# Kernel optimization log

Measured on AMD Instinct MI355X. Metric: run time of the kernel, lower is better.

## Reference

```python
import jax, jax.numpy as jnp
import numpy as np

N = 1024
D = 256            # model_dims
H = D // 2         # hidden_dim = 128
L = 3              # num_levels
EPS = 1e-5


def ln(x, g, b):
    mu = jnp.mean(x, axis=-1, keepdims=True)
    v = jnp.mean((x - mu) ** 2, axis=-1, keepdims=True)
    return (x - mu) / jnp.sqrt(v + EPS) * g + b


def setup_inputs() -> dict:
    key = jax.random.key(0)
    ks = jax.random.split(key, 24)
    s = 0.02
    inp = {
        'atomic_numbers': jax.random.randint(ks[0], (N,), 0, 100),
        'positions': jax.random.normal(ks[1], (N, 3), dtype=jnp.float32) * 3.0,
        'emb': jax.random.normal(ks[2], (100, H), dtype=jnp.float32) * s,
        # distance_expansion: Linear(3, H) + SiLU + LayerNorm(H)
        'de_W': jax.random.normal(ks[3], (L, H), dtype=jnp.float32) * s,
        'de_b': jnp.zeros((H,), jnp.float32),
        'de_g': jnp.ones((H,), jnp.float32),
        'de_be': jnp.zeros((H,), jnp.float32),
        'msg_W': jax.random.normal(ks[4], (L, 2 * H, H), dtype=jnp.float32) * s,
        'msg_b': jnp.zeros((L, H), jnp.float32),
        'msg_g': jnp.ones((L, H), jnp.float32),
        'msg_be': jnp.zeros((L, H), jnp.float32),
        'upd_W': jax.random.normal(ks[5], (L, 2 * H, H), dtype=jnp.float32) * s,
        'upd_b': jnp.zeros((L, H), jnp.float32),
        'upd_g': jnp.ones((L, H), jnp.float32),
        'upd_be': jnp.zeros((L, H), jnp.float32),
        # final proj: Linear(3H, D) + LayerNorm(D)
        'fp_W': jax.random.normal(ks[6], (L * H, D), dtype=jnp.float32) * s,
        'fp_b': jnp.zeros((D,), jnp.float32),
        'fp_g': jnp.ones((D,), jnp.float32),
        'fp_be': jnp.zeros((D,), jnp.float32),
    }
    return inp


def reference(atomic_numbers, positions, emb, de_W, de_b, de_g, de_be,
              msg_W, msg_b, msg_g, msg_be, upd_W, upd_b, upd_g, upd_be,
              fp_W, fp_b, fp_g, fp_be):
    x = emb[atomic_numbers]                                    # [N,H]
    diff = positions[:, None, :] - positions[None, :, :]       # [N,N,3]
    sq = jnp.sum(diff * diff, axis=-1)
    d = jnp.where(sq > 0, jnp.sqrt(jnp.where(sq > 0, sq, 1.0)), 0.0)  # safe norm
    scales = jnp.stack([jnp.exp(-d), jnp.exp(-d / 2), jnp.exp(-d / 4)], axis=-1)  # [N,N,3]
    ew = ln(jax.nn.silu(scales @ de_W + de_b), de_g, de_be)    # [N,N,H]

    level_feats = []
    for lvl in range(L):
        Wi, Wj = msg_W[lvl, :H], msg_W[lvl, H:]
        # cat([x_i, x_j]) @ W == x_i @ Wi + x_j @ Wj
        pre = x @ Wi                                           # [N,H]
        prj = x @ Wj                                           # [N,H]
        m = ln(jax.nn.silu(pre[:, None, :] + prj[None, :, :] + msg_b[lvl]),
               msg_g[lvl], msg_be[lvl])                        # [N,N,H]
        msum = jnp.einsum('ijh,ijh->ih', m, ew)                # sum over j
        u = jnp.concatenate([x, msum], axis=-1)                # [N,2H]
        x = x + ln(jax.nn.silu(u @ upd_W[lvl] + upd_b[lvl]), upd_g[lvl], upd_be[lvl])
        level_feats.append(jnp.mean(x, axis=0))

    combined = jnp.concatenate(level_feats, axis=0)            # [3H]
    return ln(combined @ fp_W + fp_b, fp_g, fp_be)             # [D]
```

## Files before the change

kernel.cpp:

```cpp
#include <hip/hip_runtime.h>
#include <math.h>

constexpr int N_ = 1024;
constexpr int H_ = 128;
constexpr int D_ = 256;
constexpr int L_ = 3;
constexpr float EPS_ = 1e-5f;
constexpr float LOG2E_ = 1.44269504f;
constexpr int KLUT_ = 4096;
constexpr float DMAX_ = 40.0f;
constexpr float TSCALE_ = (KLUT_ - 1) / DMAX_;
constexpr float TMAX_ = (float)(KLUT_ - 1) - 0.001f;

__device__ __forceinline__ float fsig(float v) {
    float e = __builtin_amdgcn_exp2f(v * -LOG2E_);
    return __builtin_amdgcn_rcpf(1.0f + e);
}

template <int CTRL>
__device__ __forceinline__ float rowadd(float x) {
    int y = __builtin_amdgcn_update_dpp(0, __float_as_int(x), CTRL, 0xF, 0xF, true);
    return x + __int_as_float(y);
}
__device__ __forceinline__ float rowreduce16(float x) {
    x = rowadd<0x128>(x);
    x = rowadd<0x124>(x);
    x = rowadd<0x122>(x);
    x = rowadd<0x121>(x);
    return x;
}

__device__ __forceinline__ unsigned bfr(float x) {
    unsigned u = __float_as_uint(x);
    return (u + 0x7FFFu + ((u >> 16) & 1u)) >> 16;
}

#define LD8(dst, src)                                                     \
    {                                                                     \
        float4 t0_ = *(const float4*)(src);                               \
        float4 t1_ = *(const float4*)((src) + 4);                         \
        dst[0] = t0_.x; dst[1] = t0_.y; dst[2] = t0_.z; dst[3] = t0_.w;   \
        dst[4] = t1_.x; dst[5] = t1_.y; dst[6] = t1_.z; dst[7] = t1_.w;   \
    }

__global__ void k_lut(const float* __restrict__ deW, const float* __restrict__ deb,
                      const float* __restrict__ deg, const float* __restrict__ debe,
                      unsigned* __restrict__ lutp) {
    int e = blockIdx.x * 4 + (threadIdx.x >> 6);
    int lane = threadIdx.x & 63;
    float res[2][2];
#pragma unroll
    for (int t = 0; t < 2; ++t) {
        int ee = min(e + t, KLUT_ - 1);
        float d = ee * (DMAX_ / (KLUT_ - 1));
        float s0 = expf(-d), s1 = expf(-0.5f * d), s2 = expf(-0.25f * d);
        float v[2];
        float sum = 0.f, ssq = 0.f;
#pragma unroll
        for (int kk = 0; kk < 2; ++kk) {
            int c = lane + 64 * kk;
            float a = s0 * deW[c] + s1 * deW[H_ + c] + s2 * deW[2 * H_ + c] + deb[c];
            float sg = 1.f / (1.f + expf(-a));
            v[kk] = a * sg;
            sum += v[kk]; ssq += v[kk] * v[kk];
        }
#pragma unroll
        for (int mask = 1; mask < 64; mask <<= 1) {
            sum += __shfl_xor(sum, mask);
            ssq += __shfl_xor(ssq, mask);
        }
        float mu = sum * (1.f / H_);
        float var = ssq * (1.f / H_) - mu * mu;
        float rstd = 1.f / sqrtf(var + EPS_);
#pragma unroll
        for (int kk = 0; kk < 2; ++kk) {
            int c = lane + 64 * kk;
            res[t][kk] = (v[kk] - mu) * rstd * deg[c] + debe[c];
        }
    }
#pragma unroll
    for (int kk = 0; kk < 2; ++kk) {
        int c = lane + 64 * kk;
        lutp[e * H_ + c] = bfr(res[0][kk]) | (bfr(res[1][kk] - res[0][kk]) << 16);
    }
}

__global__ void k_embed_gemm(const int* __restrict__ an, const float* __restrict__ emb,
                             const float* __restrict__ W, const float* __restrict__ b,
                             float* __restrict__ x, float* __restrict__ preb,
                             float* __restrict__ prj) {
    int i = blockIdx.x;
    int t = threadIdx.x;
    __shared__ float xr[H_];
    if (t < H_) {
        float xv = emb[an[i] * H_ + t];
        xr[t] = xv;
        x[i * H_ + t] = xv;
    }
    __syncthreads();
    int h = t & (H_ - 1);
    int off = (t >= H_) ? H_ : 0;
    float s = 0.f;
#pragma unroll 4
    for (int k = 0; k < H_; k += 4) {
        float4 xv = *(const float4*)&xr[k];
        s = fmaf(xv.x, W[(off + k) * H_ + h], s);
        s = fmaf(xv.y, W[(off + k + 1) * H_ + h], s);
        s = fmaf(xv.z, W[(off + k + 2) * H_ + h], s);
        s = fmaf(xv.w, W[(off + k + 3) * H_ + h], s);
    }
    if (t >= H_) prj[i * H_ + h] = s;
    else         preb[i * H_ + h] = s + b[h];
}

__device__ __forceinline__ void prf_step(int JT, int p, int cb, const int2* jinfo,
                                         const unsigned* __restrict__ lutp,
                                         const float* __restrict__ prjR,
                                         unsigned (&LW)[8], float (&TM)[8], float& FR) {
    int jw = (JT & (N_ - 1)) + p;
    int2 ji = jinfo[jw];
    FR = __int_as_float(ji.y);
    const unsigned* lp = (const unsigned*)((const char*)lutp + ji.x) + cb;
    uint4 a = *(const uint4*)lp;
    uint4 b = *(const uint4*)(lp + 4);
    LW[0] = a.x; LW[1] = a.y; LW[2] = a.z; LW[3] = a.w;
    LW[4] = b.x; LW[5] = b.y; LW[6] = b.z; LW[7] = b.w;
    LD8(TM, prjR + jw * H_ + cb);
}

__device__ __forceinline__ void cmp_step(const unsigned (&LW)[8], float (&TM)[8], float FR,
                                         const float (&pbv)[8], const float (&mgv)[8],
                                         const float (&mbev)[8], float (&acc)[8]) {
    float sum = 0.f, ssq = 0.f;
#pragma unroll
    for (int k = 0; k < 8; ++k) {
        float v = pbv[k] + TM[k];
        v *= fsig(v);
        TM[k] = v; sum += v; ssq = fmaf(v, v, ssq);
    }
    sum = rowreduce16(sum);
    ssq = rowreduce16(ssq);
    float mu = sum * (1.f / H_);
    float var = fmaf(ssq, 1.f / H_, -mu * mu);
    float rstd = __builtin_amdgcn_rsqf(var + EPS_);
    float c1 = -mu * rstd;
#pragma unroll
    for (int k = 0; k < 8; ++k) {
        float lo = __uint_as_float(LW[k] << 16);
        float dl = __uint_as_float(LW[k] & 0xffff0000u);
        float ew = fmaf(FR, dl, lo);
        acc[k] = fmaf(fmaf(fmaf(TM[k], rstd, c1), mgv[k], mbev[k]), ew, acc[k]);
    }
}

__global__ __launch_bounds__(512, 4) void k_pair(
    const float* __restrict__ pos, const float* __restrict__ x,
    const float* __restrict__ prebR, const float* __restrict__ prjR,
    const unsigned* __restrict__ lutp,
    const float* __restrict__ mgp, const float* __restrict__ mbep,
    const float* __restrict__ uW, const float* __restrict__ ub,
    const float* __restrict__ ug, const float* __restrict__ ube,
    const float* __restrict__ Wn, const float* __restrict__ bn,
    float* __restrict__ xout, float* __restrict__ lmean,
    float* __restrict__ prebW, float* __restrict__ prjW) {
    const int i = blockIdx.x;
    const int tid = threadIdx.x;
    const int w = tid >> 6;
    const int lane = tid & 63;
    const int g = lane >> 4;
    const int q = lane & 15;
    const int p = w * 4 + g;
    const int cb = q * 8;

    __shared__ int2 jinfo[N_];
    __shared__ float red[32][H_];
    __shared__ float msums[H_], xrow[H_], xs[H_];
    __shared__ float part[4][H_];
    __shared__ float r4[2][2];

    float pbv[8], mgv[8], mbev[8], acc[8];
    LD8(pbv, prebR + i * H_ + cb);
    LD8(mgv, mgp + cb);
    LD8(mbev, mbep + cb);
#pragma unroll
    for (int k = 0; k < 8; ++k) acc[k] = 0.f;

    const float pix = pos[3 * i], piy = pos[3 * i + 1], piz = pos[3 * i + 2];
    for (int j = tid; j < N_; j += 512) {
        float dx = pix - pos[3 * j];
        float dy = piy - pos[3 * j + 1];
        float dz = piz - pos[3 * j + 2];
        float sq = fmaf(dx, dx, fmaf(dy, dy, dz * dz));
        float d = __builtin_amdgcn_sqrtf(sq);
        float tf = fminf(d * TSCALE_, TMAX_);
        int i0 = (int)tf;
        jinfo[j] = make_int2(i0 * (H_ * 4), __float_as_int(tf - (float)i0));
    }
    if (tid < H_) xrow[tid] = x[i * H_ + tid];
    __syncthreads();

    unsigned lwA[8], lwB[8];
    float tmA[8], tmB[8], frA, frB;
    prf_step(0, p, cb, jinfo, lutp, prjR, lwA, tmA, frA);
    for (int jt = 0; jt < N_; jt += 64) {
        prf_step(jt + 32, p, cb, jinfo, lutp, prjR, lwB, tmB, frB);
        cmp_step(lwA, tmA, frA, pbv, mgv, mbev, acc);
        prf_step(jt + 64, p, cb, jinfo, lutp, prjR, lwA, tmA, frA);
        cmp_step(lwB, tmB, frB, pbv, mgv, mbev, acc);
    }

    *(float4*)&red[p][cb] = make_float4(acc[0], acc[1], acc[2], acc[3]);
    *(float4*)&red[p][cb + 4] = make_float4(acc[4], acc[5], acc[6], acc[7]);
    __syncthreads();
    if (tid < H_) {
        float s = 0.f;
#pragma unroll
        for (int pp = 0; pp < 32; ++pp) s += red[pp][tid];
        msums[tid] = s;
    }
    __syncthreads();

    int h = tid & (H_ - 1);
    int seg = tid >> 7;
    const float* src = (seg == 0) ? xrow : (seg == 1) ? xrow + 64
                     : (seg == 2) ? msums : msums + 64;
    const float* Wp = uW + (seg * 64) * H_ + h;
    float s2 = 0.f;
#pragma unroll 4
    for (int k = 0; k < 64; k += 4) {
        float4 uv = *(const float4*)&src[k];
        s2 = fmaf(uv.x, Wp[(k + 0) * H_], s2);
        s2 = fmaf(uv.y, Wp[(k + 1) * H_], s2);
        s2 = fmaf(uv.z, Wp[(k + 2) * H_], s2);
        s2 = fmaf(uv.w, Wp[(k + 3) * H_], s2);
    }
    part[seg][h] = s2;
    __syncthreads();
    float v = 0.f;
    if (tid < H_) {
        float sv = part[0][tid] + part[1][tid] + part[2][tid] + part[3][tid] + ub[tid];
        v = sv * fsig(sv);
    }
    float sum = v, ssq = v * v;
#pragma unroll
    for (int mask = 1; mask < 64; mask <<= 1) {
        sum += __shfl_xor(sum, mask);
        ssq += __shfl_xor(ssq, mask);
    }
    if (tid < H_ && (tid & 63) == 0) { r4[tid >> 6][0] = sum; r4[tid >> 6][1] = ssq; }
    __syncthreads();
    if (tid < H_) {
        sum = r4[0][0] + r4[1][0];
        ssq = r4[0][1] + r4[1][1];
        float mu = sum * (1.f / H_);
        float var = fmaf(ssq, 1.f / H_, -mu * mu);
        float rstd = rsqrtf(var + EPS_);
        float xn = xrow[tid] + fmaf((v - mu) * rstd, ug[tid], ube[tid]);
        xs[tid] = xn;
        xout[i * H_ + tid] = xn;
        atomicAdd(&lmean[tid], xn);
    }

    if (Wn) {
        __syncthreads();
        int which = tid >> 8;
        int kh = (tid >> 7) & 1;
        const float* Wp2 = Wn + (which * H_ + kh * 64) * H_ + h;
        const float* xsrc = xs + kh * 64;
        float s3 = 0.f;
#pragma unroll 4
        for (int k = 0; k < 64; k += 4) {
            float4 xv = *(const float4*)&xsrc[k];
            s3 = fmaf(xv.x, Wp2[(k + 0) * H_], s3);
            s3 = fmaf(xv.y, Wp2[(k + 1) * H_], s3);
            s3 = fmaf(xv.z, Wp2[(k + 2) * H_], s3);
            s3 = fmaf(xv.w, Wp2[(k + 3) * H_], s3);
        }
        part[(which << 1) | kh][h] = s3;
        __syncthreads();
        if (tid < 256) {
            int wh = tid >> 7, h3 = tid & 127;
            float val = part[wh * 2][h3] + part[wh * 2 + 1][h3];
            if (wh) prjW[i * H_ + h3] = val;
            else    prebW[i * H_ + h3] = val + bn[h3];
        }
    }
}

__global__ void k_final(const float* __restrict__ lmean, const float* __restrict__ fpW,
                        const float* __restrict__ fpb, const float* __restrict__ fpg,
                        const float* __restrict__ fpbe, float* __restrict__ out) {
    int t = threadIdx.x;
    __shared__ float comb[L_ * H_];
    comb[t] = lmean[t] * (1.f / N_);
    if (t < L_ * H_ - D_) comb[D_ + t] = lmean[D_ + t] * (1.f / N_);
    __syncthreads();
    float s = fpb[t];
#pragma unroll 8
    for (int k = 0; k < L_ * H_; ++k)
        s = fmaf(comb[k], fpW[k * D_ + t], s);
    float sum = s, ssq = s * s;
#pragma unroll
    for (int mask = 1; mask < 64; mask <<= 1) {
        sum += __shfl_xor(sum, mask);
        ssq += __shfl_xor(ssq, mask);
    }
    __shared__ float r4[4][2];
    int wv = t >> 6;
    if ((t & 63) == 0) { r4[wv][0] = sum; r4[wv][1] = ssq; }
    __syncthreads();
    sum = r4[0][0] + r4[1][0] + r4[2][0] + r4[3][0];
    ssq = r4[0][1] + r4[1][1] + r4[2][1] + r4[3][1];
    float mu = sum * (1.f / D_);
    float var = fmaf(ssq, 1.f / D_, -mu * mu);
    float rstd = rsqrtf(var + EPS_);
    out[t] = fmaf((s - mu) * rstd, fpg[t], fpbe[t]);
}

extern "C" void kernel_launch(void* const* d_in, const int* in_sizes, int n_in,
                              void* d_out, int out_size, void* d_ws, size_t ws_size,
                              hipStream_t stream) {
    const int*   an    = (const int*)d_in[0];
    const float* pos   = (const float*)d_in[1];
    const float* emb   = (const float*)d_in[2];
    const float* deW   = (const float*)d_in[3];
    const float* deb   = (const float*)d_in[4];
    const float* deg   = (const float*)d_in[5];
    const float* debe  = (const float*)d_in[6];
    const float* msgW  = (const float*)d_in[7];
    const float* msgb  = (const float*)d_in[8];
    const float* msgg  = (const float*)d_in[9];
    const float* msgbe = (const float*)d_in[10];
    const float* updW  = (const float*)d_in[11];
    const float* updb  = (const float*)d_in[12];
    const float* updg  = (const float*)d_in[13];
    const float* updbe = (const float*)d_in[14];
    const float* fpW   = (const float*)d_in[15];
    const float* fpb   = (const float*)d_in[16];
    const float* fpg   = (const float*)d_in[17];
    const float* fpbe  = (const float*)d_in[18];
    float* out = (float*)d_out;

    float* ws    = (float*)d_ws;
    float* x     = ws;
    float* prebA = x + N_ * H_;
    float* prjA  = prebA + N_ * H_;
    float* prebB = prjA + N_ * H_;
    float* prjB  = prebB + N_ * H_;
    float* lmean = prjB + N_ * H_;
    unsigned* lutp = (unsigned*)(lmean + L_ * H_);

    hipMemsetAsync(lmean, 0, L_ * H_ * sizeof(float), stream);
    k_lut<<<KLUT_ / 4, 256, 0, stream>>>(deW, deb, deg, debe, lutp);
    k_embed_gemm<<<N_, 256, 0, stream>>>(an, emb, msgW, msgb, x, prebA, prjA);
    for (int lvl = 0; lvl < L_; ++lvl) {
        const float* pR  = (lvl & 1) ? prebB : prebA;
        const float* prR = (lvl & 1) ? prjB  : prjA;
        float* pW  = (lvl & 1) ? prebA : prebB;
        float* prW = (lvl & 1) ? prjA  : prjB;
        const float* Wn = (lvl < L_ - 1) ? msgW + (lvl + 1) * 2 * H_ * H_ : nullptr;
        const float* bn = (lvl < L_ - 1) ? msgb + (lvl + 1) * H_ : nullptr;
        k_pair<<<N_, 512, 0, stream>>>(pos, x, pR, prR, lutp,
                                       msgg + lvl * H_, msgbe + lvl * H_,
                                       updW + lvl * 2 * H_ * H_, updb + lvl * H_,
                                       updg + lvl * H_, updbe + lvl * H_,
                                       Wn, bn, x, lmean + lvl * H_, pW, prW);
    }
    k_final<<<1, D_, 0, stream>>>(lmean, fpW, fpb, fpg, fpbe, out);
}
```

Measured before the change: 243.8 us.

## Use fp32 nearest-neighbour edge LUT and hoist LayerNorm affine out of pair loop

The edge-weight table changes from bf16 base+delta pairs with linear interpolation to a doubled-resolution fp32 table read at the nearest entry. This removes the per-element unpack and interpolation work. The LayerNorm gamma/beta multiply is factored out of the j-loop by keeping two accumulators, sum(t*ew) and sum(ew), and combining them once at the end. sched_barriers are added to pin the prefetch/compute interleave. The cost is twice the LUT bytes per gathered element and a larger table, plus a nearest-neighbour approximation error that replaces the interpolation error.

```diff
diff --git a/kernel.cpp b/kernel.cpp
--- a/kernel.cpp
+++ b/kernel.cpp
@@ -7,7 +7,7 @@
 constexpr int L_ = 3;
 constexpr float EPS_ = 1e-5f;
 constexpr float LOG2E_ = 1.44269504f;
-constexpr int KLUT_ = 4096;
+constexpr int KLUT_ = 8192;
 constexpr float DMAX_ = 40.0f;
 constexpr float TSCALE_ = (KLUT_ - 1) / DMAX_;
 constexpr float TMAX_ = (float)(KLUT_ - 1) - 0.001f;
@@ -30,11 +30,6 @@
     return x;
 }
 
-__device__ __forceinline__ unsigned bfr(float x) {
-    unsigned u = __float_as_uint(x);
-    return (u + 0x7FFFu + ((u >> 16) & 1u)) >> 16;
-}
-
 #define LD8(dst, src)                                                     \
     {                                                                     \
         float4 t0_ = *(const float4*)(src);                               \
@@ -45,43 +40,33 @@
 
 __global__ void k_lut(const float* __restrict__ deW, const float* __restrict__ deb,
                       const float* __restrict__ deg, const float* __restrict__ debe,
-                      unsigned* __restrict__ lutp) {
+                      float* __restrict__ lut) {
     int e = blockIdx.x * 4 + (threadIdx.x >> 6);
     int lane = threadIdx.x & 63;
-    float res[2][2];
-#pragma unroll
-    for (int t = 0; t < 2; ++t) {
-        int ee = min(e + t, KLUT_ - 1);
-        float d = ee * (DMAX_ / (KLUT_ - 1));
-        float s0 = expf(-d), s1 = expf(-0.5f * d), s2 = expf(-0.25f * d);
-        float v[2];
-        float sum = 0.f, ssq = 0.f;
-#pragma unroll
-        for (int kk = 0; kk < 2; ++kk) {
-            int c = lane + 64 * kk;
-            float a = s0 * deW[c] + s1 * deW[H_ + c] + s2 * deW[2 * H_ + c] + deb[c];
-            float sg = 1.f / (1.f + expf(-a));
-            v[kk] = a * sg;
-            sum += v[kk]; ssq += v[kk] * v[kk];
-        }
-#pragma unroll
-        for (int mask = 1; mask < 64; mask <<= 1) {
-            sum += __shfl_xor(sum, mask);
-            ssq += __shfl_xor(ssq, mask);
-        }
-        float mu = sum * (1.f / H_);
-        float var = ssq * (1.f / H_) - mu * mu;
-        float rstd = 1.f / sqrtf(var + EPS_);
-#pragma unroll
-        for (int kk = 0; kk < 2; ++kk) {
-            int c = lane + 64 * kk;
-            res[t][kk] = (v[kk] - mu) * rstd * deg[c] + debe[c];
-        }
-    }
+    float d = e * (DMAX_ / (KLUT_ - 1));
+    float s0 = expf(-d), s1 = expf(-0.5f * d), s2 = expf(-0.25f * d);
+    float v[2];
+    float sum = 0.f, ssq = 0.f;
 #pragma unroll
     for (int kk = 0; kk < 2; ++kk) {
         int c = lane + 64 * kk;
-        lutp[e * H_ + c] = bfr(res[0][kk]) | (bfr(res[1][kk] - res[0][kk]) << 16);
+        float a = s0 * deW[c] + s1 * deW[H_ + c] + s2 * deW[2 * H_ + c] + deb[c];
+        float sg = 1.f / (1.f + expf(-a));
+        v[kk] = a * sg;
+        sum += v[kk]; ssq += v[kk] * v[kk];
+    }
+#pragma unroll
+    for (int mask = 1; mask < 64; mask <<= 1) {
+        sum += __shfl_xor(sum, mask);
+        ssq += __shfl_xor(ssq, mask);
+    }
+    float mu = sum * (1.f / H_);
+    float var = ssq * (1.f / H_) - mu * mu;
+    float rstd = 1.f / sqrtf(var + EPS_);
+#pragma unroll
+    for (int kk = 0; kk < 2; ++kk) {
+        int c = lane + 64 * kk;
+        lut[e * H_ + c] = (v[kk] - mu) * rstd * deg[c] + debe[c];
     }
 }
 
@@ -113,30 +98,26 @@
     else         preb[i * H_ + h] = s + b[h];
 }
 
-__device__ __forceinline__ void prf_step(int JT, int p, int cb, const int2* jinfo,
-                                         const unsigned* __restrict__ lutp,
+__device__ __forceinline__ void prf_step(int JT, int p, int cb, const int* jinfo,
+                                         const float* __restrict__ lut,
                                          const float* __restrict__ prjR,
-                                         unsigned (&LW)[8], float (&TM)[8], float& FR) {
+                                         float (&EW)[8], float (&TM)[8]) {
     int jw = (JT & (N_ - 1)) + p;
-    int2 ji = jinfo[jw];
-    FR = __int_as_float(ji.y);
-    const unsigned* lp = (const unsigned*)((const char*)lutp + ji.x) + cb;
-    uint4 a = *(const uint4*)lp;
-    uint4 b = *(const uint4*)(lp + 4);
-    LW[0] = a.x; LW[1] = a.y; LW[2] = a.z; LW[3] = a.w;
-    LW[4] = b.x; LW[5] = b.y; LW[6] = b.z; LW[7] = b.w;
+    int jof = jinfo[jw];
+    const float* lp = (const float*)((const char*)lut + jof) + cb;
+    LD8(EW, lp);
     LD8(TM, prjR + jw * H_ + cb);
 }
 
-__device__ __forceinline__ void cmp_step(const unsigned (&LW)[8], float (&TM)[8], float FR,
-                                         const float (&pbv)[8], const float (&mgv)[8],
-                                         const float (&mbev)[8], float (&acc)[8]) {
+__device__ __forceinline__ void cmp_step(const float (&EW)[8], float (&TM)[8],
+                                         const float (&pbv)[8],
+                                         float (&acc1)[8], float (&acc2)[8]) {
     float sum = 0.f, ssq = 0.f;
 #pragma unroll
     for (int k = 0; k < 8; ++k) {
-        float v = pbv[k] + TM[k];
-        v *= fsig(v);
-        TM[k] = v; sum += v; ssq = fmaf(v, v, ssq);
+        float w = pbv[k] + TM[k];
+        float vv = w * fsig(w);
+        TM[k] = vv; sum += vv; ssq = fmaf(vv, vv, ssq);
     }
     sum = rowreduce16(sum);
     ssq = rowreduce16(ssq);
@@ -146,17 +127,16 @@
     float c1 = -mu * rstd;
 #pragma unroll
     for (int k = 0; k < 8; ++k) {
-        float lo = __uint_as_float(LW[k] << 16);
-        float dl = __uint_as_float(LW[k] & 0xffff0000u);
-        float ew = fmaf(FR, dl, lo);
-        acc[k] = fmaf(fmaf(fmaf(TM[k], rstd, c1), mgv[k], mbev[k]), ew, acc[k]);
+        float t = fmaf(TM[k], rstd, c1);
+        acc1[k] = fmaf(t, EW[k], acc1[k]);
+        acc2[k] += EW[k];
     }
 }
 
 __global__ __launch_bounds__(512, 4) void k_pair(
     const float* __restrict__ pos, const float* __restrict__ x,
     const float* __restrict__ prebR, const float* __restrict__ prjR,
-    const unsigned* __restrict__ lutp,
+    const float* __restrict__ lut,
     const float* __restrict__ mgp, const float* __restrict__ mbep,
     const float* __restrict__ uW, const float* __restrict__ ub,
     const float* __restrict__ ug, const float* __restrict__ ube,
@@ -172,18 +152,16 @@
     const int p = w * 4 + g;
     const int cb = q * 8;
 
-    __shared__ int2 jinfo[N_];
+    __shared__ int jinfo[N_];
     __shared__ float red[32][H_];
     __shared__ float msums[H_], xrow[H_], xs[H_];
     __shared__ float part[4][H_];
     __shared__ float r4[2][2];
 
-    float pbv[8], mgv[8], mbev[8], acc[8];
+    float pbv[8], acc1[8], acc2[8];
     LD8(pbv, prebR + i * H_ + cb);
-    LD8(mgv, mgp + cb);
-    LD8(mbev, mbep + cb);
-#pragma unroll
-    for (int k = 0; k < 8; ++k) acc[k] = 0.f;
+#pragma unroll
+    for (int k = 0; k < 8; ++k) { acc1[k] = 0.f; acc2[k] = 0.f; }
 
     const float pix = pos[3 * i], piy = pos[3 * i + 1], piz = pos[3 * i + 2];
     for (int j = tid; j < N_; j += 512) {
@@ -193,22 +171,32 @@
         float sq = fmaf(dx, dx, fmaf(dy, dy, dz * dz));
         float d = __builtin_amdgcn_sqrtf(sq);
         float tf = fminf(d * TSCALE_, TMAX_);
-        int i0 = (int)tf;
-        jinfo[j] = make_int2(i0 * (H_ * 4), __float_as_int(tf - (float)i0));
+        int i0 = (int)(tf + 0.5f);
+        jinfo[j] = i0 * (H_ * 4);
     }
     if (tid < H_) xrow[tid] = x[i * H_ + tid];
     __syncthreads();
 
-    unsigned lwA[8], lwB[8];
-    float tmA[8], tmB[8], frA, frB;
-    prf_step(0, p, cb, jinfo, lutp, prjR, lwA, tmA, frA);
+    float ewA[8], tmA[8], ewB[8], tmB[8];
+    prf_step(0, p, cb, jinfo, lut, prjR, ewA, tmA);
+    __builtin_amdgcn_sched_barrier(0);
     for (int jt = 0; jt < N_; jt += 64) {
-        prf_step(jt + 32, p, cb, jinfo, lutp, prjR, lwB, tmB, frB);
-        cmp_step(lwA, tmA, frA, pbv, mgv, mbev, acc);
-        prf_step(jt + 64, p, cb, jinfo, lutp, prjR, lwA, tmA, frA);
-        cmp_step(lwB, tmB, frB, pbv, mgv, mbev, acc);
-    }
-
+        prf_step(jt + 32, p, cb, jinfo, lut, prjR, ewB, tmB);
+        __builtin_amdgcn_sched_barrier(0);
+        cmp_step(ewA, tmA, pbv, acc1, acc2);
+        __builtin_amdgcn_sched_barrier(0);
+        prf_step(jt + 64, p, cb, jinfo, lut, prjR, ewA, tmA);
+        __builtin_amdgcn_sched_barrier(0);
+        cmp_step(ewB, tmB, pbv, acc1, acc2);
+        __builtin_amdgcn_sched_barrier(0);
+    }
+
+    float mgv[8], mbev[8], acc[8];
+    LD8(mgv, mgp + cb);
+    LD8(mbev, mbep + cb);
+#pragma unroll
+    for (int k = 0; k < 8; ++k)
+        acc[k] = mgv[k] * acc1[k] + mbev[k] * acc2[k];
     *(float4*)&red[p][cb] = make_float4(acc[0], acc[1], acc[2], acc[3]);
     *(float4*)&red[p][cb + 4] = make_float4(acc[4], acc[5], acc[6], acc[7]);
     __syncthreads();
@@ -348,10 +336,10 @@
     float* prebB = prjA + N_ * H_;
     float* prjB  = prebB + N_ * H_;
     float* lmean = prjB + N_ * H_;
-    unsigned* lutp = (unsigned*)(lmean + L_ * H_);
+    float* lut   = lmean + L_ * H_;
 
     hipMemsetAsync(lmean, 0, L_ * H_ * sizeof(float), stream);
-    k_lut<<<KLUT_ / 4, 256, 0, stream>>>(deW, deb, deg, debe, lutp);
+    k_lut<<<KLUT_ / 4, 256, 0, stream>>>(deW, deb, deg, debe, lut);
     k_embed_gemm<<<N_, 256, 0, stream>>>(an, emb, msgW, msgb, x, prebA, prjA);
     for (int lvl = 0; lvl < L_; ++lvl) {
         const float* pR  = (lvl & 1) ? prebB : prebA;
@@ -360,7 +348,7 @@
         float* prW = (lvl & 1) ? prjA  : prjB;
         const float* Wn = (lvl < L_ - 1) ? msgW + (lvl + 1) * 2 * H_ * H_ : nullptr;
         const float* bn = (lvl < L_ - 1) ? msgb + (lvl + 1) * H_ : nullptr;
-        k_pair<<<N_, 512, 0, stream>>>(pos, x, pR, prR, lutp,
+        k_pair<<<N_, 512, 0, stream>>>(pos, x, pR, prR, lut,
                                        msgg + lvl * H_, msgbe + lvl * H_,
                                        updW + lvl * 2 * H_ * H_, updb + lvl * H_,
                                        updg + lvl * H_, updbe + lvl * H_,
```

New measurement: 234.4 us. -3.8%, faster.
